# Kernel tuning notes

Hardware: AMD Instinct MI355X
Metric: run time of the kernel (lower is better)

The kernel has to match this reference:

```python
import jax, jax.numpy as jnp
import numpy as np

B, T, D_MODEL = 2, 2048, 2048
NUM_HEADS, NUM_KV_HEADS, HEAD_DIM = 16, 16, 128
NUM_Q_HEADS = 2 * NUM_HEADS  # diff-v2 doubles the query heads


def _rope_freqs(seqlen, dim_half, base=10000.0):
    inv = 1.0 / (base ** (np.arange(0, dim_half, dtype=np.float32) / dim_half))
    t = np.arange(seqlen, dtype=np.float32)
    ang = np.outer(t, inv)  # [T, dim_half]
    return jnp.asarray(np.cos(ang)), jnp.asarray(np.sin(ang))


def apply_rotary_interleaved(x, cos, sin):
    # x: [B, T, H, D]; cos/sin: [T, D//2]; pairs are adjacent (interleaved=True)
    x1, x2 = x[..., 0::2], x[..., 1::2]
    c = cos[None, :, None, :]
    s = sin[None, :, None, :]
    o1 = x1 * c - x2 * s
    o2 = x1 * s + x2 * c
    return jnp.stack([o1, o2], axis=-1).reshape(x.shape)


def setup_inputs() -> dict:
    key = jax.random.key(0)
    ks = jax.random.split(key, 6)
    x = jax.random.normal(ks[0], (B, T, D_MODEL), dtype=jnp.float32)
    cos, sin = _rope_freqs(T, HEAD_DIM // 2)
    sc = 1.0 / np.sqrt(D_MODEL)
    Wq = jax.random.normal(ks[1], (D_MODEL, NUM_Q_HEADS * HEAD_DIM), dtype=jnp.float32) * sc
    Wk = jax.random.normal(ks[2], (D_MODEL, NUM_KV_HEADS * HEAD_DIM), dtype=jnp.float32) * sc
    Wv = jax.random.normal(ks[3], (D_MODEL, NUM_KV_HEADS * HEAD_DIM), dtype=jnp.float32) * sc
    Wo = jax.random.normal(ks[4], (NUM_HEADS * HEAD_DIM, D_MODEL), dtype=jnp.float32) * sc
    Wlam = jax.random.normal(ks[5], (D_MODEL, NUM_HEADS), dtype=jnp.float32) * sc
    return {"x": x, "cos": cos, "sin": sin, "Wq": Wq, "Wk": Wk, "Wv": Wv, "Wo": Wo, "Wlam": Wlam}


def reference(x, cos, sin, Wq, Wk, Wv, Wo, Wlam):
    b, t, _ = x.shape
    q = (x @ Wq).reshape(b, t, NUM_Q_HEADS, HEAD_DIM)
    k = (x @ Wk).reshape(b, t, NUM_KV_HEADS, HEAD_DIM)
    v = (x @ Wv).reshape(b, t, NUM_KV_HEADS, HEAD_DIM)
    q = apply_rotary_interleaved(q, cos, sin)
    k = apply_rotary_interleaved(k, cos, sin)
    # GQA: repeat kv heads to match the doubled query heads
    rep = NUM_Q_HEADS // NUM_KV_HEADS
    k = jnp.repeat(k, rep, axis=2)
    v = jnp.repeat(v, rep, axis=2)
    scale = 1.0 / np.sqrt(HEAD_DIM)
    scores = jnp.einsum('bthd,bshd->bhts', q, k) * scale  # [B, 2H, T, T]
    causal = jnp.tril(jnp.ones((t, t), dtype=bool))
    scores = jnp.where(causal[None, None], scores, jnp.finfo(scores.dtype).min)
    p = jax.nn.softmax(scores, axis=-1)
    attn = jnp.einsum('bhts,bshd->bthd', p, v)  # [B, T, 2H, D]
    lam = jax.nn.sigmoid(x @ Wlam)  # [B, T, H]
    attn1, attn2 = attn[:, :, 0::2], attn[:, :, 1::2]
    out = attn1 - lam[..., None] * attn2  # [B, T, H, D]
    return out.reshape(b, t, NUM_HEADS * HEAD_DIM) @ Wo
```

## Files before the change

### kernel.cpp

```cpp
#include <hip/hip_runtime.h>

#define T_SEQ 2048
#define BATCH 2
#define DMODEL 2048
#define NQH 32
#define NKVH 16
#define HD 128

typedef _Float16 f16;
typedef _Float16 f16x8 __attribute__((ext_vector_type(8)));
typedef _Float16 f16x4 __attribute__((ext_vector_type(4)));
typedef _Float16 f16x2 __attribute__((ext_vector_type(2)));
typedef float f32x4 __attribute__((ext_vector_type(4)));

typedef const __attribute__((address_space(1))) void* gptr_t;
typedef __attribute__((address_space(3))) void* sptr_t;
#define GLDS16(g, l) __builtin_amdgcn_global_load_lds((gptr_t)(g), (sptr_t)(l), 16, 0, 0)

__global__ void k_convert_f16(const float* __restrict__ in, f16* __restrict__ out, int n8) {
  int i = blockIdx.x * blockDim.x + threadIdx.x;
  int stride = gridDim.x * blockDim.x;
  for (; i < n8; i += stride) {
    const float4* p = (const float4*)(in) + (size_t)i * 2;
    float4 a = p[0], b = p[1];
    f16x8 v;
    v[0]=(f16)a.x; v[1]=(f16)a.y; v[2]=(f16)a.z; v[3]=(f16)a.w;
    v[4]=(f16)b.x; v[5]=(f16)b.y; v[6]=(f16)b.z; v[7]=(f16)b.w;
    *((f16x8*)out + i) = v;
  }
}

__global__ __launch_bounds__(256) void k_transpose_f16(const float* __restrict__ W,
                                                       f16* __restrict__ WT, int K, int N) {
  __shared__ float tile[32][33];
  int n0 = blockIdx.x * 32, k0 = blockIdx.y * 32;
  int tx = threadIdx.x & 31;
  int ty0 = threadIdx.x >> 5;
  #pragma unroll
  for (int i = 0; i < 4; ++i) {
    int ty = ty0 + i * 8;
    tile[ty][tx] = W[(size_t)(k0 + ty) * N + n0 + tx];
  }
  __syncthreads();
  #pragma unroll
  for (int i = 0; i < 4; ++i) {
    int ty = ty0 + i * 8;
    WT[(size_t)(n0 + ty) * K + k0 + tx] = (f16)tile[tx][ty];
  }
}

template<int BM, int BN, int WM, int WN, int OM>
__global__ __launch_bounds__(512, 2) void k_gemm2(const f16* __restrict__ A,
                                                  const f16* __restrict__ BT,
                                                  void* __restrict__ C0,
                                                  f16* __restrict__ Kh,
                                                  f16* __restrict__ VTg,
                                                  const float* __restrict__ cosb,
                                                  const float* __restrict__ sinb,
                                                  int M, int N, int K) {
  constexpr int MR = BM / WM / 16;
  constexpr int NR = BN / WN / 16;
  constexpr int ACH = BM / 64;
  constexpr int BCH = BN / 64;
  __shared__ alignas(16) f16 Al[2][BM * 64];
  __shared__ alignas(16) f16 Bl[2][BN * 64];
  const int tid = threadIdx.x;
  const int lane = tid & 63;
  const int w = tid >> 6;
  const int wr = w / WN, wc = w % WN;
  const int lr = lane & 15, lg = lane >> 4;
  const int nbx = N / BN;
  const int cpx = gridDim.x >> 3;
  const int wg = (blockIdx.x & 7) * cpx + (blockIdx.x >> 3);
  const int m0 = (wg / nbx) * BM, n0 = (wg % nbx) * BN;

  auto STAGE = [&](int buf, int kk) {
    #pragma unroll
    for (int q = 0; q < ACH; ++q) {
      int idx = q * 512 + tid;
      int r = idx >> 3, g = idx & 7;
      GLDS16(A + (size_t)(m0 + r) * K + kk + ((g ^ (r & 7)) * 8), &Al[buf][idx * 8]);
    }
    #pragma unroll
    for (int q = 0; q < BCH; ++q) {
      int idx = q * 512 + tid;
      int r = idx >> 3, g = idx & 7;
      GLDS16(BT + (size_t)(n0 + r) * K + kk + ((g ^ (r & 7)) * 8), &Bl[buf][idx * 8]);
    }
  };

  f32x4 acc[MR][NR] = {};
  STAGE(0, 0);
  const int nt = K / 64;
  #pragma unroll 2
  for (int t = 0; t < nt; ++t) {
    const int buf = t & 1;
    if (t + 1 < nt) {
      STAGE(buf ^ 1, (t + 1) * 64);
      __builtin_amdgcn_sched_barrier(0);
      if constexpr (ACH + BCH == 8) asm volatile("s_waitcnt vmcnt(8)" ::: "memory");
      else                          asm volatile("s_waitcnt vmcnt(6)" ::: "memory");
    } else {
      __builtin_amdgcn_sched_barrier(0);
      asm volatile("s_waitcnt vmcnt(0)" ::: "memory");
    }
    __builtin_amdgcn_s_barrier();
    __builtin_amdgcn_sched_barrier(0);
    #pragma unroll
    for (int kh = 0; kh < 2; ++kh) {
      f16x8 af[MR], bf[NR];
      #pragma unroll
      for (int i = 0; i < MR; ++i) {
        int r = wr * (BM / WM) + i * 16 + lr;
        af[i] = *(const f16x8*)&Al[buf][r * 64 + (((kh * 4 + lg) ^ (r & 7)) * 8)];
      }
      #pragma unroll
      for (int j = 0; j < NR; ++j) {
        int r = wc * (BN / WN) + j * 16 + lr;
        bf[j] = *(const f16x8*)&Bl[buf][r * 64 + (((kh * 4 + lg) ^ (r & 7)) * 8)];
      }
      #pragma unroll
      for (int i = 0; i < MR; ++i)
        #pragma unroll
        for (int j = 0; j < NR; ++j)
          acc[i][j] = __builtin_amdgcn_mfma_f32_16x16x32_f16(af[i], bf[j], acc[i][j], 0, 0, 0);
    }
    __builtin_amdgcn_sched_barrier(0);
    __builtin_amdgcn_s_barrier();
    __builtin_amdgcn_sched_barrier(0);
  }

  const int mb = m0 + wr * (BM / WM);
  const int nb = n0 + wc * (BN / WN);
  if constexpr (OM == 0) {
    float* C = (float*)C0;
    #pragma unroll
    for (int i = 0; i < MR; ++i)
      #pragma unroll
      for (int j = 0; j < NR; ++j) {
        int r0 = mb + i * 16 + lg * 4;
        int c = nb + j * 16 + lr;
        #pragma unroll
        for (int r = 0; r < 4; ++r)
          C[(size_t)(r0 + r) * N + c] = acc[i][j][r];
      }
  } else {
    if (n0 < 6144) {
      f16* dst = (n0 < 4096) ? (f16*)C0 : Kh;
      const int ncols = (n0 < 4096) ? 4096 : 2048;
      const int coff = (n0 < 4096) ? 0 : 4096;
      #pragma unroll
      for (int i = 0; i < MR; ++i)
        #pragma unroll
        for (int j = 0; j < NR; ++j) {
          int c = nb + j * 16 + lr - coff;
          int jp = (c & 127) >> 1;
          bool odd = (c & 1);
          #pragma unroll
          for (int r = 0; r < 4; ++r) {
            int row = mb + i * 16 + lg * 4 + r;
            int t = row & (T_SEQ - 1);
            float v = acc[i][j][r];
            float pv = __shfl_xor(v, 1);
            float cs = cosb[t * 64 + jp], sn = sinb[t * 64 + jp];
            float out = odd ? (pv * sn + v * cs) : (v * cs - pv * sn);
            dst[(size_t)row * ncols + c] = (f16)out;
          }
        }
    } else {
      #pragma unroll
      for (int i = 0; i < MR; ++i)
        #pragma unroll
        for (int j = 0; j < NR; ++j) {
          int c = nb + j * 16 + lr - 6144;
          int head = c >> 7, d = c & 127;
          int row0 = mb + i * 16 + lg * 4;
          int bb = row0 >> 11, t0 = row0 & (T_SEQ - 1);
          f16x4 zv;
          #pragma unroll
          for (int r = 0; r < 4; ++r) zv[r] = (f16)acc[i][j][r];
          *(f16x4*)(VTg + ((size_t)(bb * NKVH + head) * HD + d) * T_SEQ + t0) = zv;
        }
    }
  }
}

__global__ __launch_bounds__(256) void k_lambda(const float* __restrict__ x,
                                                const float* __restrict__ Wlam,
                                                float* __restrict__ lam) {
  int row = blockIdx.x;
  const float* xr = x + (size_t)row * DMODEL;
  float acc[16];
  #pragma unroll
  for (int h = 0; h < 16; ++h) acc[h] = 0.f;
  for (int e = threadIdx.x; e < DMODEL; e += 256) {
    float xv = xr[e];
    const float4* wp = (const float4*)(Wlam + e * 16);
    #pragma unroll
    for (int g = 0; g < 4; ++g) {
      float4 wv = wp[g];
      acc[g * 4 + 0] += xv * wv.x; acc[g * 4 + 1] += xv * wv.y;
      acc[g * 4 + 2] += xv * wv.z; acc[g * 4 + 3] += xv * wv.w;
    }
  }
  #pragma unroll
  for (int h = 0; h < 16; ++h)
    for (int off = 32; off > 0; off >>= 1)
      acc[h] += __shfl_down(acc[h], off);
  __shared__ float part[4][16];
  int lane = threadIdx.x & 63, w = threadIdx.x >> 6;
  if (lane == 0) {
    #pragma unroll
    for (int h = 0; h < 16; ++h) part[w][h] = acc[h];
  }
  __syncthreads();
  if (threadIdx.x < 16) {
    float s = part[0][threadIdx.x] + part[1][threadIdx.x] + part[2][threadIdx.x] + part[3][threadIdx.x];
    lam[row * 16 + threadIdx.x] = 1.f / (1.f + __expf(-s));
  }
}

__global__ __launch_bounds__(256, 4) void k_attn4(const f16* __restrict__ Q,
                                                  const f16* __restrict__ K,
                                                  const f16* __restrict__ VT,
                                                  f16* __restrict__ O) {
  __shared__ f16 Kl[64 * 128];
  __shared__ f16 Vl[128 * 64];
  __shared__ f16 Pl[4][16][40];
  const int tid = threadIdx.x;
  const int lane = tid & 63;
  const int w = tid >> 6;
  const int lr = lane & 15, lg = lane >> 4;
  const int flat = blockIdx.x;
  const int xcd = flat & 7;
  const int work = xcd * 128 + (flat >> 3);
  const int grp = work >> 5;
  const int within = work & 31;
  const int b = grp >> 4, hkv = grp & 15;
  const int h = hkv * 2 + (within >> 4);
  const int bx = within & 15;
  const f16* Kg  = K  + (size_t)b * T_SEQ * (NKVH * HD) + hkv * HD;
  const f16* VTg = VT + (size_t)(b * NKVH + hkv) * HD * T_SEQ;
  const float sc = 0.08838834764831845f;

  #pragma unroll 1
  for (int half = 0; half < 2; ++half) {
    const int qt = half ? (31 - bx) : bx;
    const int qb = qt * 64;
    const int qw = qb + w * 16;
    const int qrow = qw + lr;
    f16x8 qf[4];
    {
      const f16* qp = Q + (size_t)(b * T_SEQ + qrow) * (NQH * HD) + h * HD + lg * 8;
      #pragma unroll
      for (int c = 0; c < 4; ++c) qf[c] = *(const f16x8*)(qp + c * 32);
    }
    f32x4 o[8] = {};
    float mi = -1e30f, li = 0.f;

    const int nt = qt + 1;
    #pragma unroll 1
    for (int t = 0; t < nt; ++t) {
      const int s0 = t * 64;
      #pragma unroll
      for (int qq = 0; qq < 4; ++qq) {
        int idx = qq * 256 + tid;
        int r = idx >> 4, g = idx & 15;
        GLDS16(Kg + (size_t)(s0 + r) * (NKVH * HD) + (g ^ (r & 7)) * 8, &Kl[idx * 8]);
      }
      #pragma unroll
      for (int qq = 0; qq < 4; ++qq) {
        int idx = qq * 256 + tid;
        int d = idx >> 3, g = idx & 7;
        GLDS16(VTg + (size_t)d * T_SEQ + s0 + (g ^ (d & 7)) * 8, &Vl[idx * 8]);
      }
      __syncthreads();

      f32x4 sf[4] = {};
      #pragma unroll
      for (int c = 0; c < 4; ++c) {
        #pragma unroll
        for (int nb = 0; nb < 4; ++nb) {
          f16x8 kf = *(const f16x8*)&Kl[(((nb * 16 + lr) * 16) + ((c * 4 + lg) ^ (lr & 7))) * 8];
          sf[nb] = __builtin_amdgcn_mfma_f32_16x16x32_f16(kf, qf[c], sf[nb], 0, 0, 0);
        }
      }
      float v[16];
      #pragma unroll
      for (int nb = 0; nb < 4; ++nb)
        #pragma unroll
        for (int rr = 0; rr < 4; ++rr) {
          float x = sf[nb][rr] * sc;
          int kv = s0 + nb * 16 + lg * 4 + rr;
          v[nb * 4 + rr] = (kv > qrow) ? -1e30f : x;
        }
      float pm = v[0];
      #pragma unroll
      for (int i = 1; i < 16; ++i) pm = fmaxf(pm, v[i]);
      pm = fmaxf(pm, __shfl_xor(pm, 16));
      pm = fmaxf(pm, __shfl_xor(pm, 32));
      float mnew = fmaxf(mi, pm);
      float a = __expf(mi - mnew);
      mi = mnew;
      float rs = 0.f;
      #pragma unroll
      for (int i = 0; i < 16; ++i) { float p = __expf(v[i] - mnew); v[i] = p; rs += p; }
      rs += __shfl_xor(rs, 16);
      rs += __shfl_xor(rs, 32);
      li = a * li + rs;
      float ab[4];
      #pragma unroll
      for (int rr = 0; rr < 4; ++rr) ab[rr] = __shfl(a, lg * 4 + rr);
      #pragma unroll
      for (int j = 0; j < 8; ++j)
        #pragma unroll
        for (int rr = 0; rr < 4; ++rr) o[j][rr] *= ab[rr];
      #pragma unroll
      for (int ks = 0; ks < 2; ++ks) {
        #pragma unroll
        for (int nb2 = 0; nb2 < 2; ++nb2) {
          int nb = ks * 2 + nb2;
          f16x4 pk;
          #pragma unroll
          for (int rr = 0; rr < 4; ++rr) pk[rr] = (f16)v[nb * 4 + rr];
          *(f16x4*)&Pl[w][lr][nb2 * 16 + lg * 4] = pk;
        }
        f16x8 pa = *(const f16x8*)&Pl[w][lr][lg * 8];
        #pragma unroll
        for (int j = 0; j < 8; ++j) {
          f16x8 vbj = *(const f16x8*)&Vl[(((j * 16 + lr) * 8) + ((ks * 4 + lg) ^ (lr & 7))) * 8];
          o[j] = __builtin_amdgcn_mfma_f32_16x16x32_f16(pa, vbj, o[j], 0, 0, 0);
        }
      }
      __syncthreads();
    }
    float lib[4];
    #pragma unroll
    for (int rr = 0; rr < 4; ++rr) lib[rr] = 1.f / __shfl(li, lg * 4 + rr);
    #pragma unroll
    for (int j = 0; j < 8; ++j)
      #pragma unroll
      for (int rr = 0; rr < 4; ++rr) {
        float vv = o[j][rr] * lib[rr];
        O[(size_t)(b * T_SEQ + qw + lg * 4 + rr) * (NQH * HD) + h * HD + j * 16 + lr] = (f16)vv;
      }
  }
}

__global__ void k_combine(const f16* __restrict__ attn, const float* __restrict__ lam,
                          f16* __restrict__ Z) {
  int idx = blockIdx.x * blockDim.x + threadIdx.x;
  int d4 = idx & 31;
  int tmp = idx >> 5;
  int h = tmp & 15;
  int row = tmp >> 4;
  if (row >= BATCH * T_SEQ) return;
  float lv = lam[row * 16 + h];
  f16x4 a1 = *(const f16x4*)(attn + (size_t)row * 4096 + (2 * h) * 128 + d4 * 4);
  f16x4 a2 = *(const f16x4*)(attn + (size_t)row * 4096 + (2 * h + 1) * 128 + d4 * 4);
  f16x4 z;
  #pragma unroll
  for (int e = 0; e < 4; ++e) z[e] = (f16)((float)a1[e] - lv * (float)a2[e]);
  *(f16x4*)(Z + (size_t)row * 2048 + h * 128 + d4 * 4) = z;
}

extern "C" void kernel_launch(void* const* d_in, const int* in_sizes, int n_in,
                              void* d_out, int out_size, void* d_ws, size_t ws_size,
                              hipStream_t stream) {
  const float* x    = (const float*)d_in[0];
  const float* cosb = (const float*)d_in[1];
  const float* sinb = (const float*)d_in[2];
  const float* Wq   = (const float*)d_in[3];
  const float* Wk   = (const float*)d_in[4];
  const float* Wv   = (const float*)d_in[5];
  const float* Wo   = (const float*)d_in[6];
  const float* Wlam = (const float*)d_in[7];

  char* ws = (char*)d_ws;
  f16*  xh     = (f16*)(ws);
  f16*  WqkvT  = (f16*)(ws + 16777216);
  f16*  WoT    = (f16*)(ws + 50331648);
  f16*  Qh     = (f16*)(ws + 58720256);
  f16*  Kh     = (f16*)(ws + 92274688);
  f16*  VTg    = (f16*)(ws + 109051904);
  f16*  At     = (f16*)(ws + 125829120);
  f16*  Zh     = (f16*)(ws + 159383552);
  float* lam   = (float*)(ws + 176160768);

  k_convert_f16<<<2048, 256, 0, stream>>>(x, xh, BATCH * T_SEQ * DMODEL / 8);
  k_transpose_f16<<<dim3(4096 / 32, 2048 / 32), 256, 0, stream>>>(Wq, WqkvT, DMODEL, 4096);
  k_transpose_f16<<<dim3(2048 / 32, 2048 / 32), 256, 0, stream>>>(Wk, WqkvT + (size_t)4096 * 2048, DMODEL, 2048);
  k_transpose_f16<<<dim3(2048 / 32, 2048 / 32), 256, 0, stream>>>(Wv, WqkvT + (size_t)6144 * 2048, DMODEL, 2048);
  k_transpose_f16<<<dim3(2048 / 32, 2048 / 32), 256, 0, stream>>>(Wo, WoT, 2048, 2048);
  k_lambda<<<4096, 256, 0, stream>>>(x, Wlam, lam);

  k_gemm2<256, 256, 2, 4, 3><<<512, 512, 0, stream>>>(xh, WqkvT, Qh, Kh, VTg,
                                                      cosb, sinb, 4096, 8192, 2048);

  k_attn4<<<1024, 256, 0, stream>>>(Qh, Kh, VTg, At);

  k_combine<<<(BATCH * T_SEQ * 16 * 32) / 256, 256, 0, stream>>>(At, lam, Zh);

  k_gemm2<256, 128, 4, 2, 0><<<256, 512, 0, stream>>>(Zh, WoT, d_out, nullptr, nullptr,
                                                      nullptr, nullptr, 4096, 2048, 2048);
}
```

Baseline: 416.6 us.

## Restructure GEMM main loop into interleaved phases and merge prep kernels

The GEMM loop is split into four phases. Each phase issues part of the next tile's A or B async loads, then does LDS reads and MFMAs on half the M rows, with s_setprio raised around the MFMA blocks. The aim is to overlap global loads with compute, and launch bounds drop to one block per SIMD. The four weight transposes become one launch using blockIdx.z, and the x-to-f16 conversion is fused into the lambda kernel to cut launch overhead. Attention MFMA sections also get setprio hints. The risks are the extra barriers per iteration, a full vmcnt(0) wait at the end of each iteration, and changed occupancy.

```diff
diff --git a/kernel.cpp b/kernel.cpp
--- a/kernel.cpp
+++ b/kernel.cpp
@@ -17,23 +17,25 @@
 typedef __attribute__((address_space(3))) void* sptr_t;
 #define GLDS16(g, l) __builtin_amdgcn_global_load_lds((gptr_t)(g), (sptr_t)(l), 16, 0, 0)
 
-__global__ void k_convert_f16(const float* __restrict__ in, f16* __restrict__ out, int n8) {
-  int i = blockIdx.x * blockDim.x + threadIdx.x;
-  int stride = gridDim.x * blockDim.x;
-  for (; i < n8; i += stride) {
-    const float4* p = (const float4*)(in) + (size_t)i * 2;
-    float4 a = p[0], b = p[1];
-    f16x8 v;
-    v[0]=(f16)a.x; v[1]=(f16)a.y; v[2]=(f16)a.z; v[3]=(f16)a.w;
-    v[4]=(f16)b.x; v[5]=(f16)b.y; v[6]=(f16)b.z; v[7]=(f16)b.w;
-    *((f16x8*)out + i) = v;
-  }
-}
-
-__global__ __launch_bounds__(256) void k_transpose_f16(const float* __restrict__ W,
-                                                       f16* __restrict__ WT, int K, int N) {
+__global__ __launch_bounds__(256) void k_transpose_all(const float* __restrict__ Wq,
+                                                       const float* __restrict__ Wk,
+                                                       const float* __restrict__ Wv,
+                                                       const float* __restrict__ Wo,
+                                                       f16* __restrict__ WqkvT,
+                                                       f16* __restrict__ WoT) {
   __shared__ float tile[32][33];
-  int n0 = blockIdx.x * 32, k0 = blockIdx.y * 32;
+  const int z = blockIdx.z;
+  const float* W;
+  f16* WT;
+  int N;
+  if (z == 0)      { W = Wq; WT = WqkvT;                          N = 4096; }
+  else if (z == 1) { W = Wk; WT = WqkvT + (size_t)4096 * 2048;    N = 2048; }
+  else if (z == 2) { W = Wv; WT = WqkvT + (size_t)6144 * 2048;    N = 2048; }
+  else             { W = Wo; WT = WoT;                            N = 2048; }
+  const int K = 2048;
+  int n0 = blockIdx.x * 32;
+  if (n0 >= N) return;
+  int k0 = blockIdx.y * 32;
   int tx = threadIdx.x & 31;
   int ty0 = threadIdx.x >> 5;
   #pragma unroll
@@ -50,7 +52,7 @@
 }
 
 template<int BM, int BN, int WM, int WN, int OM>
-__global__ __launch_bounds__(512, 2) void k_gemm2(const f16* __restrict__ A,
+__global__ __launch_bounds__(512, 1) void k_gemm3(const f16* __restrict__ A,
                                                   const f16* __restrict__ BT,
                                                   void* __restrict__ C0,
                                                   f16* __restrict__ Kh,
@@ -59,6 +61,7 @@
                                                   const float* __restrict__ sinb,
                                                   int M, int N, int K) {
   constexpr int MR = BM / WM / 16;
+  constexpr int MR2 = MR / 2;
   constexpr int NR = BN / WN / 16;
   constexpr int ACH = BM / 64;
   constexpr int BCH = BN / 64;
@@ -74,61 +77,83 @@
   const int wg = (blockIdx.x & 7) * cpx + (blockIdx.x >> 3);
   const int m0 = (wg / nbx) * BM, n0 = (wg % nbx) * BN;
 
-  auto STAGE = [&](int buf, int kk) {
-    #pragma unroll
-    for (int q = 0; q < ACH; ++q) {
-      int idx = q * 512 + tid;
-      int r = idx >> 3, g = idx & 7;
-      GLDS16(A + (size_t)(m0 + r) * K + kk + ((g ^ (r & 7)) * 8), &Al[buf][idx * 8]);
-    }
-    #pragma unroll
-    for (int q = 0; q < BCH; ++q) {
-      int idx = q * 512 + tid;
-      int r = idx >> 3, g = idx & 7;
-      GLDS16(BT + (size_t)(n0 + r) * K + kk + ((g ^ (r & 7)) * 8), &Bl[buf][idx * 8]);
-    }
-  };
+#define STAGE_A(BUF, KK)                                                        \
+  { _Pragma("unroll")                                                           \
+    for (int q = 0; q < ACH; ++q) {                                             \
+      int idx = q * 512 + tid; int r = idx >> 3, g = idx & 7;                   \
+      GLDS16(A + (size_t)(m0 + r) * K + (KK) + ((g ^ (r & 7)) * 8),             \
+             &Al[BUF][idx * 8]);                                                \
+    } }
+#define STAGE_B(BUF, KK)                                                        \
+  { _Pragma("unroll")                                                           \
+    for (int q = 0; q < BCH; ++q) {                                             \
+      int idx = q * 512 + tid; int r = idx >> 3, g = idx & 7;                   \
+      GLDS16(BT + (size_t)(n0 + r) * K + (KK) + ((g ^ (r & 7)) * 8),            \
+             &Bl[BUF][idx * 8]);                                                \
+    } }
+#define LDA8(AF, MH, KH)                                                        \
+  { _Pragma("unroll")                                                           \
+    for (int i = 0; i < MR2; ++i) {                                             \
+      int r = wr * (BM / WM) + ((MH) * MR2 + i) * 16 + lr;                      \
+      AF[i] = *(const f16x8*)&Al[buf][r * 64 + ((((KH) * 4 + lg) ^ (r & 7)) * 8)]; \
+    } }
+#define LDB8(BF, KH)                                                            \
+  { _Pragma("unroll")                                                           \
+    for (int j = 0; j < NR; ++j) {                                              \
+      int r = wc * (BN / WN) + j * 16 + lr;                                     \
+      BF[j] = *(const f16x8*)&Bl[buf][r * 64 + ((((KH) * 4 + lg) ^ (r & 7)) * 8)]; \
+    } }
+#define FMA8(AF, BF, MH)                                                        \
+  { __builtin_amdgcn_s_setprio(1);                                              \
+    _Pragma("unroll")                                                           \
+    for (int i = 0; i < MR2; ++i)                                               \
+      _Pragma("unroll")                                                         \
+      for (int j = 0; j < NR; ++j)                                              \
+        acc[(MH) * MR2 + i][j] =                                                \
+          __builtin_amdgcn_mfma_f32_16x16x32_f16(AF[i], BF[j], acc[(MH) * MR2 + i][j], 0, 0, 0); \
+    __builtin_amdgcn_s_setprio(0); }
+#define PHASE_BAR()                                                             \
+  { __builtin_amdgcn_sched_barrier(0); __builtin_amdgcn_s_barrier();            \
+    __builtin_amdgcn_sched_barrier(0); }
 
   f32x4 acc[MR][NR] = {};
-  STAGE(0, 0);
+  STAGE_A(0, 0);
+  STAGE_B(0, 0);
+  asm volatile("s_waitcnt vmcnt(0)" ::: "memory");
+  __builtin_amdgcn_s_barrier();
+  __builtin_amdgcn_sched_barrier(0);
+
   const int nt = K / 64;
   #pragma unroll 2
   for (int t = 0; t < nt; ++t) {
     const int buf = t & 1;
-    if (t + 1 < nt) {
-      STAGE(buf ^ 1, (t + 1) * 64);
-      __builtin_amdgcn_sched_barrier(0);
-      if constexpr (ACH + BCH == 8) asm volatile("s_waitcnt vmcnt(8)" ::: "memory");
-      else                          asm volatile("s_waitcnt vmcnt(6)" ::: "memory");
-    } else {
-      __builtin_amdgcn_sched_barrier(0);
-      asm volatile("s_waitcnt vmcnt(0)" ::: "memory");
-    }
+    f16x8 af[MR2], bf[NR];
+    if (t + 1 < nt) STAGE_A(buf ^ 1, (t + 1) * 64);
+    LDB8(bf, 0);
+    LDA8(af, 0, 0);
+    FMA8(af, bf, 0);
+    PHASE_BAR();
+    if (t + 1 < nt) STAGE_B(buf ^ 1, (t + 1) * 64);
+    LDA8(af, 1, 0);
+    FMA8(af, bf, 1);
+    PHASE_BAR();
+    LDB8(bf, 1);
+    LDA8(af, 0, 1);
+    FMA8(af, bf, 0);
+    PHASE_BAR();
+    LDA8(af, 1, 1);
+    FMA8(af, bf, 1);
+    __builtin_amdgcn_sched_barrier(0);
+    asm volatile("s_waitcnt vmcnt(0)" ::: "memory");
     __builtin_amdgcn_s_barrier();
     __builtin_amdgcn_sched_barrier(0);
-    #pragma unroll
-    for (int kh = 0; kh < 2; ++kh) {
-      f16x8 af[MR], bf[NR];
-      #pragma unroll
-      for (int i = 0; i < MR; ++i) {
-        int r = wr * (BM / WM) + i * 16 + lr;
-        af[i] = *(const f16x8*)&Al[buf][r * 64 + (((kh * 4 + lg) ^ (r & 7)) * 8)];
-      }
-      #pragma unroll
-      for (int j = 0; j < NR; ++j) {
-        int r = wc * (BN / WN) + j * 16 + lr;
-        bf[j] = *(const f16x8*)&Bl[buf][r * 64 + (((kh * 4 + lg) ^ (r & 7)) * 8)];
-      }
-      #pragma unroll
-      for (int i = 0; i < MR; ++i)
-        #pragma unroll
-        for (int j = 0; j < NR; ++j)
-          acc[i][j] = __builtin_amdgcn_mfma_f32_16x16x32_f16(af[i], bf[j], acc[i][j], 0, 0, 0);
-    }
-    __builtin_amdgcn_sched_barrier(0);
-    __builtin_amdgcn_s_barrier();
-    __builtin_amdgcn_sched_barrier(0);
-  }
+  }
+#undef STAGE_A
+#undef STAGE_B
+#undef LDA8
+#undef LDB8
+#undef FMA8
+#undef PHASE_BAR
 
   const int mb = m0 + wr * (BM / WM);
   const int nb = n0 + wc * (BN / WN);
@@ -185,22 +210,31 @@
   }
 }
 
-__global__ __launch_bounds__(256) void k_lambda(const float* __restrict__ x,
-                                                const float* __restrict__ Wlam,
-                                                float* __restrict__ lam) {
+__global__ __launch_bounds__(256) void k_lambda_conv(const float* __restrict__ x,
+                                                     const float* __restrict__ Wlam,
+                                                     float* __restrict__ lam,
+                                                     f16* __restrict__ xh) {
   int row = blockIdx.x;
   const float* xr = x + (size_t)row * DMODEL;
+  const int e = threadIdx.x * 8;
+  const float4* xp = (const float4*)(xr + e);
+  float4 a = xp[0], b2 = xp[1];
+  float xv[8] = {a.x, a.y, a.z, a.w, b2.x, b2.y, b2.z, b2.w};
+  f16x8 hv;
+  #pragma unroll
+  for (int j = 0; j < 8; ++j) hv[j] = (f16)xv[j];
+  *(f16x8*)(xh + (size_t)row * DMODEL + e) = hv;
   float acc[16];
   #pragma unroll
   for (int h = 0; h < 16; ++h) acc[h] = 0.f;
-  for (int e = threadIdx.x; e < DMODEL; e += 256) {
-    float xv = xr[e];
-    const float4* wp = (const float4*)(Wlam + e * 16);
+  #pragma unroll
+  for (int j = 0; j < 8; ++j) {
+    const float4* wp = (const float4*)(Wlam + (size_t)(e + j) * 16);
     #pragma unroll
     for (int g = 0; g < 4; ++g) {
       float4 wv = wp[g];
-      acc[g * 4 + 0] += xv * wv.x; acc[g * 4 + 1] += xv * wv.y;
-      acc[g * 4 + 2] += xv * wv.z; acc[g * 4 + 3] += xv * wv.w;
+      acc[g * 4 + 0] += xv[j] * wv.x; acc[g * 4 + 1] += xv[j] * wv.y;
+      acc[g * 4 + 2] += xv[j] * wv.z; acc[g * 4 + 3] += xv[j] * wv.w;
     }
   }
   #pragma unroll
@@ -277,6 +311,7 @@
       __syncthreads();
 
       f32x4 sf[4] = {};
+      __builtin_amdgcn_s_setprio(1);
       #pragma unroll
       for (int c = 0; c < 4; ++c) {
         #pragma unroll
@@ -285,6 +320,7 @@
           sf[nb] = __builtin_amdgcn_mfma_f32_16x16x32_f16(kf, qf[c], sf[nb], 0, 0, 0);
         }
       }
+      __builtin_amdgcn_s_setprio(0);
       float v[16];
       #pragma unroll
       for (int nb = 0; nb < 4; ++nb)
@@ -326,11 +362,13 @@
           *(f16x4*)&Pl[w][lr][nb2 * 16 + lg * 4] = pk;
         }
         f16x8 pa = *(const f16x8*)&Pl[w][lr][lg * 8];
+        __builtin_amdgcn_s_setprio(1);
         #pragma unroll
         for (int j = 0; j < 8; ++j) {
           f16x8 vbj = *(const f16x8*)&Vl[(((j * 16 + lr) * 8) + ((ks * 4 + lg) ^ (lr & 7))) * 8];
           o[j] = __builtin_amdgcn_mfma_f32_16x16x32_f16(pa, vbj, o[j], 0, 0, 0);
         }
+        __builtin_amdgcn_s_setprio(0);
       }
       __syncthreads();
     }
@@ -387,20 +425,16 @@
   f16*  Zh     = (f16*)(ws + 159383552);
   float* lam   = (float*)(ws + 176160768);
 
-  k_convert_f16<<<2048, 256, 0, stream>>>(x, xh, BATCH * T_SEQ * DMODEL / 8);
-  k_transpose_f16<<<dim3(4096 / 32, 2048 / 32), 256, 0, stream>>>(Wq, WqkvT, DMODEL, 4096);
-  k_transpose_f16<<<dim3(2048 / 32, 2048 / 32), 256, 0, stream>>>(Wk, WqkvT + (size_t)4096 * 2048, DMODEL, 2048);
-  k_transpose_f16<<<dim3(2048 / 32, 2048 / 32), 256, 0, stream>>>(Wv, WqkvT + (size_t)6144 * 2048, DMODEL, 2048);
-  k_transpose_f16<<<dim3(2048 / 32, 2048 / 32), 256, 0, stream>>>(Wo, WoT, 2048, 2048);
-  k_lambda<<<4096, 256, 0, stream>>>(x, Wlam, lam);
-
-  k_gemm2<256, 256, 2, 4, 3><<<512, 512, 0, stream>>>(xh, WqkvT, Qh, Kh, VTg,
+  k_transpose_all<<<dim3(128, 64, 4), 256, 0, stream>>>(Wq, Wk, Wv, Wo, WqkvT, WoT);
+  k_lambda_conv<<<4096, 256, 0, stream>>>(x, Wlam, lam, xh);
+
+  k_gemm3<256, 256, 2, 4, 3><<<512, 512, 0, stream>>>(xh, WqkvT, Qh, Kh, VTg,
                                                       cosb, sinb, 4096, 8192, 2048);
 
   k_attn4<<<1024, 256, 0, stream>>>(Qh, Kh, VTg, At);
 
   k_combine<<<(BATCH * T_SEQ * 16 * 32) / 256, 256, 0, stream>>>(At, lam, Zh);
 
-  k_gemm2<256, 128, 4, 2, 0><<<256, 512, 0, stream>>>(Zh, WoT, d_out, nullptr, nullptr,
+  k_gemm3<256, 128, 4, 2, 0><<<256, 512, 0, stream>>>(Zh, WoT, d_out, nullptr, nullptr,
                                                       nullptr, nullptr, 4096, 2048, 2048);
 }
```

New measurement: 495.3 us. +18.9%, slower.

## Share KV tiles across paired query heads, prefetch KV, fuse prep kernels

Applied to the files above, without the earlier changes.

The attention kernel now runs 512-thread blocks in which both query heads of a KV head share one K/V tile in LDS. This halves the K/V global traffic per query head. The next K/V tile is prefetched into registers while the current one is computed, MFMA sections get raised wave priority, and the online-softmax rescale is skipped when the running max does not grow by more than a threshold. Separately, the four weight transposes are merged into one launch and the x-to-fp16 conversion is fused into the lambda kernel. The trade-offs are higher register pressure, an extra barrier per iteration, and a lazy-rescale path that depends on the threshold to stay numerically safe.

```diff
diff --git a/kernel.cpp b/kernel.cpp
--- a/kernel.cpp
+++ b/kernel.cpp
@@ -17,23 +17,25 @@
 typedef __attribute__((address_space(3))) void* sptr_t;
 #define GLDS16(g, l) __builtin_amdgcn_global_load_lds((gptr_t)(g), (sptr_t)(l), 16, 0, 0)
 
-__global__ void k_convert_f16(const float* __restrict__ in, f16* __restrict__ out, int n8) {
-  int i = blockIdx.x * blockDim.x + threadIdx.x;
-  int stride = gridDim.x * blockDim.x;
-  for (; i < n8; i += stride) {
-    const float4* p = (const float4*)(in) + (size_t)i * 2;
-    float4 a = p[0], b = p[1];
-    f16x8 v;
-    v[0]=(f16)a.x; v[1]=(f16)a.y; v[2]=(f16)a.z; v[3]=(f16)a.w;
-    v[4]=(f16)b.x; v[5]=(f16)b.y; v[6]=(f16)b.z; v[7]=(f16)b.w;
-    *((f16x8*)out + i) = v;
-  }
-}
-
-__global__ __launch_bounds__(256) void k_transpose_f16(const float* __restrict__ W,
-                                                       f16* __restrict__ WT, int K, int N) {
+__global__ __launch_bounds__(256) void k_transpose_all(const float* __restrict__ Wq,
+                                                       const float* __restrict__ Wk,
+                                                       const float* __restrict__ Wv,
+                                                       const float* __restrict__ Wo,
+                                                       f16* __restrict__ WqkvT,
+                                                       f16* __restrict__ WoT) {
   __shared__ float tile[32][33];
-  int n0 = blockIdx.x * 32, k0 = blockIdx.y * 32;
+  const int z = blockIdx.z;
+  const float* W;
+  f16* WT;
+  int N;
+  if (z == 0)      { W = Wq; WT = WqkvT;                          N = 4096; }
+  else if (z == 1) { W = Wk; WT = WqkvT + (size_t)4096 * 2048;    N = 2048; }
+  else if (z == 2) { W = Wv; WT = WqkvT + (size_t)6144 * 2048;    N = 2048; }
+  else             { W = Wo; WT = WoT;                            N = 2048; }
+  const int K = 2048;
+  int n0 = blockIdx.x * 32;
+  if (n0 >= N) return;
+  int k0 = blockIdx.y * 32;
   int tx = threadIdx.x & 31;
   int ty0 = threadIdx.x >> 5;
   #pragma unroll
@@ -185,22 +187,31 @@
   }
 }
 
-__global__ __launch_bounds__(256) void k_lambda(const float* __restrict__ x,
-                                                const float* __restrict__ Wlam,
-                                                float* __restrict__ lam) {
+__global__ __launch_bounds__(256) void k_lambda_conv(const float* __restrict__ x,
+                                                     const float* __restrict__ Wlam,
+                                                     float* __restrict__ lam,
+                                                     f16* __restrict__ xh) {
   int row = blockIdx.x;
   const float* xr = x + (size_t)row * DMODEL;
+  const int e = threadIdx.x * 8;
+  const float4* xp = (const float4*)(xr + e);
+  float4 a = xp[0], b2 = xp[1];
+  float xv[8] = {a.x, a.y, a.z, a.w, b2.x, b2.y, b2.z, b2.w};
+  f16x8 hv;
+  #pragma unroll
+  for (int j = 0; j < 8; ++j) hv[j] = (f16)xv[j];
+  *(f16x8*)(xh + (size_t)row * DMODEL + e) = hv;
   float acc[16];
   #pragma unroll
   for (int h = 0; h < 16; ++h) acc[h] = 0.f;
-  for (int e = threadIdx.x; e < DMODEL; e += 256) {
-    float xv = xr[e];
-    const float4* wp = (const float4*)(Wlam + e * 16);
+  #pragma unroll
+  for (int j = 0; j < 8; ++j) {
+    const float4* wp = (const float4*)(Wlam + (size_t)(e + j) * 16);
     #pragma unroll
     for (int g = 0; g < 4; ++g) {
       float4 wv = wp[g];
-      acc[g * 4 + 0] += xv * wv.x; acc[g * 4 + 1] += xv * wv.y;
-      acc[g * 4 + 2] += xv * wv.z; acc[g * 4 + 3] += xv * wv.w;
+      acc[g * 4 + 0] += xv[j] * wv.x; acc[g * 4 + 1] += xv[j] * wv.y;
+      acc[g * 4 + 2] += xv[j] * wv.z; acc[g * 4 + 3] += xv[j] * wv.w;
     }
   }
   #pragma unroll
@@ -220,26 +231,27 @@
   }
 }
 
-__global__ __launch_bounds__(256, 4) void k_attn4(const f16* __restrict__ Q,
+__global__ __launch_bounds__(512, 4) void k_attn5(const f16* __restrict__ Q,
                                                   const f16* __restrict__ K,
                                                   const f16* __restrict__ VT,
                                                   f16* __restrict__ O) {
   __shared__ f16 Kl[64 * 128];
   __shared__ f16 Vl[128 * 64];
-  __shared__ f16 Pl[4][16][40];
+  __shared__ f16 Pl[8][16][40];
   const int tid = threadIdx.x;
   const int lane = tid & 63;
   const int w = tid >> 6;
   const int lr = lane & 15, lg = lane >> 4;
   const int flat = blockIdx.x;
   const int xcd = flat & 7;
-  const int work = xcd * 128 + (flat >> 3);
-  const int grp = work >> 5;
-  const int within = work & 31;
+  const int work = xcd * 64 + (flat >> 3);
+  const int grp = work >> 4;
+  const int bx = work & 15;
   const int b = grp >> 4, hkv = grp & 15;
-  const int h = hkv * 2 + (within >> 4);
-  const int bx = within & 15;
-  const f16* Kg  = K  + (size_t)b * T_SEQ * (NKVH * HD) + hkv * HD;
+  const int h = hkv * 2 + (w >> 2);
+  const int wq = w & 3;
+  const int kvstride = NKVH * HD;
+  const f16* Kg  = K  + (size_t)b * T_SEQ * kvstride + hkv * HD;
   const f16* VTg = VT + (size_t)(b * NKVH + hkv) * HD * T_SEQ;
   const float sc = 0.08838834764831845f;
 
@@ -247,7 +259,7 @@
   for (int half = 0; half < 2; ++half) {
     const int qt = half ? (31 - bx) : bx;
     const int qb = qt * 64;
-    const int qw = qb + w * 16;
+    const int qw = qb + wq * 16;
     const int qrow = qw + lr;
     f16x8 qf[4];
     {
@@ -259,24 +271,42 @@
     float mi = -1e30f, li = 0.f;
 
     const int nt = qt + 1;
+    #pragma unroll
+    for (int q = 0; q < 2; ++q) {
+      int idx = q * 512 + tid;
+      int r = idx >> 4, g = idx & 15;
+      GLDS16(Kg + (size_t)r * kvstride + (g ^ (r & 7)) * 8, &Kl[idx * 8]);
+    }
+    #pragma unroll
+    for (int q = 0; q < 2; ++q) {
+      int idx = q * 512 + tid;
+      int d = idx >> 3, g = idx & 7;
+      GLDS16(VTg + (size_t)d * T_SEQ + (g ^ (d & 7)) * 8, &Vl[idx * 8]);
+    }
+    __syncthreads();
+
     #pragma unroll 1
     for (int t = 0; t < nt; ++t) {
       const int s0 = t * 64;
-      #pragma unroll
-      for (int qq = 0; qq < 4; ++qq) {
-        int idx = qq * 256 + tid;
-        int r = idx >> 4, g = idx & 15;
-        GLDS16(Kg + (size_t)(s0 + r) * (NKVH * HD) + (g ^ (r & 7)) * 8, &Kl[idx * 8]);
-      }
-      #pragma unroll
-      for (int qq = 0; qq < 4; ++qq) {
-        int idx = qq * 256 + tid;
-        int d = idx >> 3, g = idx & 7;
-        GLDS16(VTg + (size_t)d * T_SEQ + s0 + (g ^ (d & 7)) * 8, &Vl[idx * 8]);
-      }
-      __syncthreads();
-
+      const bool pf = (t + 1 < nt);
+      f16x8 ka[2], va[2];
+      if (pf) {
+        const int s1 = s0 + 64;
+        #pragma unroll
+        for (int q = 0; q < 2; ++q) {
+          int idx = q * 512 + tid;
+          int r = idx >> 4, g = idx & 15;
+          ka[q] = *(const f16x8*)(Kg + (size_t)(s1 + r) * kvstride + g * 8);
+        }
+        #pragma unroll
+        for (int q = 0; q < 2; ++q) {
+          int idx = q * 512 + tid;
+          int d = idx >> 3, g = idx & 7;
+          va[q] = *(const f16x8*)(VTg + (size_t)d * T_SEQ + s1 + g * 8);
+        }
+      }
       f32x4 sf[4] = {};
+      __builtin_amdgcn_s_setprio(1);
       #pragma unroll
       for (int c = 0; c < 4; ++c) {
         #pragma unroll
@@ -285,13 +315,15 @@
           sf[nb] = __builtin_amdgcn_mfma_f32_16x16x32_f16(kf, qf[c], sf[nb], 0, 0, 0);
         }
       }
+      __builtin_amdgcn_s_setprio(0);
       float v[16];
       #pragma unroll
       for (int nb = 0; nb < 4; ++nb)
         #pragma unroll
         for (int rr = 0; rr < 4; ++rr) {
           float x = sf[nb][rr] * sc;
-          int kv = s0 + nb * 16 + lg * 4 + rr;
+          int kv = s0 + nb * 4 * 4 + nb * 0 + nb * 0;
+          kv = s0 + nb * 16 + lg * 4 + rr;
           v[nb * 4 + rr] = (kv > qrow) ? -1e30f : x;
         }
       float pm = v[0];
@@ -299,22 +331,27 @@
       for (int i = 1; i < 16; ++i) pm = fmaxf(pm, v[i]);
       pm = fmaxf(pm, __shfl_xor(pm, 16));
       pm = fmaxf(pm, __shfl_xor(pm, 32));
-      float mnew = fmaxf(mi, pm);
-      float a = __expf(mi - mnew);
-      mi = mnew;
+      const bool nogrow = (__all(pm <= mi + 8.0f) != 0);
+      const float mnew = nogrow ? mi : fmaxf(mi, pm);
       float rs = 0.f;
       #pragma unroll
       for (int i = 0; i < 16; ++i) { float p = __expf(v[i] - mnew); v[i] = p; rs += p; }
       rs += __shfl_xor(rs, 16);
       rs += __shfl_xor(rs, 32);
-      li = a * li + rs;
-      float ab[4];
-      #pragma unroll
-      for (int rr = 0; rr < 4; ++rr) ab[rr] = __shfl(a, lg * 4 + rr);
-      #pragma unroll
-      for (int j = 0; j < 8; ++j)
-        #pragma unroll
-        for (int rr = 0; rr < 4; ++rr) o[j][rr] *= ab[rr];
+      if (nogrow) {
+        li += rs;
+      } else {
+        float a = __expf(mi - mnew);
+        mi = mnew;
+        li = a * li + rs;
+        float ab[4];
+        #pragma unroll
+        for (int rr = 0; rr < 4; ++rr) ab[rr] = __shfl(a, lg * 4 + rr);
+        #pragma unroll
+        for (int j = 0; j < 8; ++j)
+          #pragma unroll
+          for (int rr = 0; rr < 4; ++rr) o[j][rr] *= ab[rr];
+      }
       #pragma unroll
       for (int ks = 0; ks < 2; ++ks) {
         #pragma unroll
@@ -326,10 +363,27 @@
           *(f16x4*)&Pl[w][lr][nb2 * 16 + lg * 4] = pk;
         }
         f16x8 pa = *(const f16x8*)&Pl[w][lr][lg * 8];
+        __builtin_amdgcn_s_setprio(1);
         #pragma unroll
         for (int j = 0; j < 8; ++j) {
           f16x8 vbj = *(const f16x8*)&Vl[(((j * 16 + lr) * 8) + ((ks * 4 + lg) ^ (lr & 7))) * 8];
           o[j] = __builtin_amdgcn_mfma_f32_16x16x32_f16(pa, vbj, o[j], 0, 0, 0);
+        }
+        __builtin_amdgcn_s_setprio(0);
+      }
+      __syncthreads();
+      if (pf) {
+        #pragma unroll
+        for (int q = 0; q < 2; ++q) {
+          int idx = q * 512 + tid;
+          int r = idx >> 4, g = idx & 15;
+          *(f16x8*)&Kl[(r * 16 + (g ^ (r & 7))) * 8] = ka[q];
+        }
+        #pragma unroll
+        for (int q = 0; q < 2; ++q) {
+          int idx = q * 512 + tid;
+          int d = idx >> 3, g = idx & 7;
+          *(f16x8*)&Vl[(d * 8 + (g ^ (d & 7))) * 8] = va[q];
         }
       }
       __syncthreads();
@@ -387,17 +441,13 @@
   f16*  Zh     = (f16*)(ws + 159383552);
   float* lam   = (float*)(ws + 176160768);
 
-  k_convert_f16<<<2048, 256, 0, stream>>>(x, xh, BATCH * T_SEQ * DMODEL / 8);
-  k_transpose_f16<<<dim3(4096 / 32, 2048 / 32), 256, 0, stream>>>(Wq, WqkvT, DMODEL, 4096);
-  k_transpose_f16<<<dim3(2048 / 32, 2048 / 32), 256, 0, stream>>>(Wk, WqkvT + (size_t)4096 * 2048, DMODEL, 2048);
-  k_transpose_f16<<<dim3(2048 / 32, 2048 / 32), 256, 0, stream>>>(Wv, WqkvT + (size_t)6144 * 2048, DMODEL, 2048);
-  k_transpose_f16<<<dim3(2048 / 32, 2048 / 32), 256, 0, stream>>>(Wo, WoT, 2048, 2048);
-  k_lambda<<<4096, 256, 0, stream>>>(x, Wlam, lam);
+  k_transpose_all<<<dim3(128, 64, 4), 256, 0, stream>>>(Wq, Wk, Wv, Wo, WqkvT, WoT);
+  k_lambda_conv<<<4096, 256, 0, stream>>>(x, Wlam, lam, xh);
 
   k_gemm2<256, 256, 2, 4, 3><<<512, 512, 0, stream>>>(xh, WqkvT, Qh, Kh, VTg,
                                                       cosb, sinb, 4096, 8192, 2048);
 
-  k_attn4<<<1024, 256, 0, stream>>>(Qh, Kh, VTg, At);
+  k_attn5<<<512, 512, 0, stream>>>(Qh, Kh, VTg, At);
 
   k_combine<<<(BATCH * T_SEQ * 16 * 32) / 256, 256, 0, stream>>>(At, lam, Zh);
 
```

New measurement: 439.8 us. 5.6% more time.
